# Kernel tuning notes

Measured on AMD Instinct MI355X. Metric: run time of the kernel, lower is better.

## Reference

```python
import jax, jax.numpy as jnp
import numpy as np

N, E, F_IN, HID, HEADS, NCLS, NG = 50000, 800000, 128, 128, 4, 10, 512
C = HID // HEADS          # per-head channels
BN_EPS = 1e-5
NEG_SLOPE = 0.2           # SuperGATConv default negative_slope
N_CONV = 3


def setup_inputs() -> dict:
    key = jax.random.key(0)
    ks = jax.random.split(key, 16)
    x = jax.random.normal(ks[0], (N, F_IN), jnp.float32)
    # edges with no self loops (reference appends self loops itself, as SuperGATConv does)
    src = jax.random.randint(ks[1], (E,), 0, N, dtype=jnp.int32)
    off = jax.random.randint(ks[2], (E,), 1, N, dtype=jnp.int32)
    dst = (src + off) % N
    edge_index = jnp.stack([src, dst], axis=0)
    batch = jnp.sort(jax.random.randint(ks[3], (N,), 0, NG, dtype=jnp.int32))
    s = 0.1
    # BatchNorm params per module init: weight=1, bias=1e-4 (running stats fresh: mean=0, var=1)
    inp = {
        "x": x, "edge_index": edge_index, "batch": batch,
        "bn_feat_g": jnp.ones((F_IN,), jnp.float32), "bn_feat_b": jnp.full((F_IN,), 1e-4, jnp.float32),
        "w_feat": jax.random.normal(ks[4], (F_IN, HID), jnp.float32) * s,
        "b_feat": jnp.zeros((HID,), jnp.float32),
        "bn_conv_g": jnp.ones((N_CONV, HID), jnp.float32), "bn_conv_b": jnp.full((N_CONV, HID), 1e-4, jnp.float32),
        "w_gat": jax.random.normal(ks[5], (N_CONV, HID, HID), jnp.float32) * s,
        "att_l": jax.random.normal(ks[6], (N_CONV, HEADS, C), jnp.float32) * s,
        "att_r": jax.random.normal(ks[7], (N_CONV, HEADS, C), jnp.float32) * s,
        "b_gat": jnp.zeros((N_CONV, HID), jnp.float32),
        "bn_fc_g": jnp.ones((HID,), jnp.float32), "bn_fc_b": jnp.full((HID,), 1e-4, jnp.float32),
        "w_fc": jax.random.normal(ks[8], (HID, HID), jnp.float32) * s,
        "b_fc": jnp.zeros((HID,), jnp.float32),
        "bn_hid_g": jnp.ones((HID,), jnp.float32), "bn_hid_b": jnp.full((HID,), 1e-4, jnp.float32),
        "w_cls": jax.random.normal(ks[9], (HID, NCLS), jnp.float32) * s,
        "b_cls": jnp.zeros((NCLS,), jnp.float32),
    }
    return inp


def _bn_eval(h, g, b):
    # eval-mode BatchNorm1d with fresh running stats (mean=0, var=1)
    return h * (g / jnp.sqrt(1.0 + BN_EPS)) + b


def _segment_softmax(a, seg, num_segments):
    # softmax over edges grouped by destination node (PyG softmax semantics)
    m = jax.ops.segment_max(a, seg, num_segments=num_segments)
    a = jnp.exp(a - m[seg])
    s = jax.ops.segment_sum(a, seg, num_segments=num_segments)
    return a / (s[seg] + 1e-16)


def _supergat_mx(h, src, dst, W, att_l, att_r, bias):
    # h: [N, HID] -> per-head features [N, H, C]
    hh = (h @ W).reshape(N, HEADS, C)
    h_j = hh[src]  # source (message) features  [E2, H, C]
    h_i = hh[dst]  # destination features       [E2, H, C]
    logits = jnp.einsum('ehc,ehc->eh', h_i, h_j)                       # MX dot-product
    alpha = jnp.einsum('ehc,hc->eh', h_j, att_l) + jnp.einsum('ehc,hc->eh', h_i, att_r)
    alpha = alpha * jax.nn.sigmoid(logits)
    alpha = jax.nn.leaky_relu(alpha, NEG_SLOPE)
    alpha = _segment_softmax(alpha, dst, N)                            # [E2, H]
    out = jax.ops.segment_sum(h_j * alpha[..., None], dst, num_segments=N)
    return out.reshape(N, HID) + bias


def reference(x, edge_index, batch, bn_feat_g, bn_feat_b, w_feat, b_feat,
              bn_conv_g, bn_conv_b, w_gat, att_l, att_r, b_gat,
              bn_fc_g, bn_fc_b, w_fc, b_fc, bn_hid_g, bn_hid_b, w_cls, b_cls):
    loops = jnp.arange(N, dtype=edge_index.dtype)
    src = jnp.concatenate([edge_index[0], loops])   # SuperGATConv adds self loops
    dst = jnp.concatenate([edge_index[1], loops])
    h = _bn_eval(x, bn_feat_g, bn_feat_b)
    h = jax.nn.relu(h @ w_feat + b_feat)            # GCNConv(gfn=True) == Linear
    for i in range(N_CONV):
        h = _bn_eval(h, bn_conv_g[i], bn_conv_b[i])
        h = jax.nn.relu(_supergat_mx(h, src, dst, w_gat[i], att_l[i], att_r[i], b_gat[i]))
    g = jax.ops.segment_sum(h, batch, num_segments=NG)  # global_add_pool -> [NG, HID]
    g = _bn_eval(g, bn_fc_g, bn_fc_b)
    g = jax.nn.relu(g @ w_fc + b_fc)
    g = _bn_eval(g, bn_hid_g, bn_hid_b)
    logits = g @ w_cls + b_cls
    att_loss = jnp.float32(0.0)  # eval mode: no edge-sampled attention loss
    return jax.nn.log_softmax(logits, axis=-1), att_loss
```

## Files before the change

### kernel.cpp

```cpp
#include <hip/hip_runtime.h>

#define NN 50000
#define EE 800000
#define FHID 128
#define NHEAD 4
#define NGRAPH 512
#define NCLS 10
#define BK 256
#define BCH 4096
#define NBLK_E 196
#define NBUCK 196
#define CAP 6144

typedef unsigned short u16;
typedef unsigned int u32;
typedef unsigned long long u64;
typedef __attribute__((ext_vector_type(8))) short bf16x8;
typedef __attribute__((ext_vector_type(4))) float f32x4;

__device__ __forceinline__ float bf2f(u16 u){
    union { u32 i; float f; } v; v.i = ((u32)u) << 16; return v.f;
}
__device__ __forceinline__ float bflo(u32 u){
    union { u32 i; float f; } v; v.i = u << 16; return v.f;
}
__device__ __forceinline__ float bfhi(u32 u){
    union { u32 i; float f; } v; v.i = u & 0xffff0000u; return v.f;
}
__device__ __forceinline__ u16 f2bf(float f){
    union { float f; u32 i; } v; v.f = f;
    u32 r = v.i + 0x7fffu + ((v.i >> 16) & 1u);
    return (u16)(r >> 16);
}
__device__ __forceinline__ u32 pack2(float a, float b){
    return ((u32)f2bf(b) << 16) | f2bf(a);
}
__device__ __forceinline__ float loadF(const void* p, int i, int isf32){
    return isf32 ? ((const float*)p)[i] : bf2f(((const u16*)p)[i]);
}
__device__ __forceinline__ void unpk8(uint4 v, float* f){
    f[0]=bflo(v.x); f[1]=bfhi(v.x);
    f[2]=bflo(v.y); f[3]=bfhi(v.y);
    f[4]=bflo(v.z); f[5]=bfhi(v.z);
    f[6]=bflo(v.w); f[7]=bfhi(v.w);
}

__global__ void detect_dtype(const u16* __restrict__ x, int* __restrict__ flag){
    __shared__ int cnt;
    if (threadIdx.x == 0) cnt = 0;
    __syncthreads();
    int ok = 0;
    for (int i = threadIdx.x; i < 1024; i += 256){
        u16 u = x[i];
        int e = (u >> 7) & 0xFF;
        if ((u & 0x7fff) == 0 || (e >= 0x70 && e <= 0x85)) ok++;
    }
    atomicAdd(&cnt, ok);
    __syncthreads();
    if (threadIdx.x == 0) flag[0] = (cnt < 900) ? 1 : 0;
}

__global__ void prep_weights(const void* __restrict__ w_feat, const void* __restrict__ b_feat,
                             const void* __restrict__ bn_feat_g, const void* __restrict__ bn_feat_b,
                             const void* __restrict__ w_gat, const void* __restrict__ bn_conv_g,
                             const void* __restrict__ bn_conv_b, const void* __restrict__ b_gat,
                             const int* __restrict__ flag,
                             u16* __restrict__ Wt, float* __restrict__ cvec,
                             float* __restrict__ biasv)
{
    __shared__ float red[128];
    int isf32 = flag[0];
    int L = blockIdx.x >> 7;
    int n = blockIdx.x & 127;
    int k = threadIdx.x;
    const float rs = rsqrtf(1.0f + 1e-5f);
    float wv, bg, bb;
    if (L == 0){
        wv = loadF(w_feat, k*FHID + n, isf32);
        bg = loadF(bn_feat_g, k, isf32);
        bb = loadF(bn_feat_b, k, isf32);
    } else {
        wv = loadF(w_gat, (L-1)*FHID*FHID + k*FHID + n, isf32);
        bg = loadF(bn_conv_g, (L-1)*FHID + k, isf32);
        bb = loadF(bn_conv_b, (L-1)*FHID + k, isf32);
    }
    Wt[L*FHID*FHID + n*FHID + k] = f2bf(bg * rs * wv);
    red[k] = bb * wv;
    __syncthreads();
    for (int o2 = 64; o2 > 0; o2 >>= 1){
        if (k < o2) red[k] += red[k + o2];
        __syncthreads();
    }
    if (k == 0){
        float c = red[0];
        if (L == 0) c += loadF(b_feat, n, isf32);
        cvec[L*FHID + n] = c;
        if (L > 0) biasv[L*FHID + n] = loadF(b_gat, (L-1)*FHID + n, isf32);
    }
}

__global__ void prep_head(const void* wfc, const void* bfc, const void* bnfg, const void* bnfb,
                          const void* bnhg, const void* bnhb, const void* wcls, const void* bcls,
                          const void* attl, const void* attr,
                          const int* __restrict__ flag, float* __restrict__ hp){
    int isf32 = flag[0];
    int gt = blockIdx.x*256 + threadIdx.x;
    for (int i = gt; i < FHID*FHID; i += 16*256) hp[i] = loadF(wfc, i, isf32);
    if (gt < FHID*NCLS) hp[16384 + gt] = loadF(wcls, gt, isf32);
    if (gt >= 2048 && gt < 2048 + 3*FHID){
        int i = gt - 2048;
        hp[18320 + i] = loadF(attl, i, isf32);
        hp[18704 + i] = loadF(attr, i, isf32);
    }
    if (gt >= 2560 && gt < 2560 + FHID){
        int t = gt - 2560;
        hp[17664 + t] = loadF(bnfg, t, isf32);
        hp[17792 + t] = loadF(bnfb, t, isf32);
        hp[17920 + t] = loadF(bfc,  t, isf32);
        hp[18048 + t] = loadF(bnhg, t, isf32);
        hp[18176 + t] = loadF(bnhb, t, isf32);
    }
    if (gt >= 3072 && gt < 3072 + NCLS) hp[18304 + (gt - 3072)] = loadF(bcls, gt - 3072, isf32);
}

__global__ __launch_bounds__(256) void gemm128(const void* __restrict__ A,
                                               const u16* __restrict__ Wt,
                                               const float* __restrict__ cvec,
                                               u16* __restrict__ out, int relu,
                                               int araw, const int* __restrict__ flag)
{
    int wave = threadIdx.x >> 6;
    int lane = threadIdx.x & 63;
    int m = lane & 15, quad = lane >> 4;
    int rowbase = blockIdx.x * 128 + wave * 32;
    bool f32in = araw && flag[0];
    const u16*  Au = (const u16*)A;
    const float* Af = (const float*)A;
    int r0 = rowbase + m, r1 = rowbase + 16 + m;
    bool v0 = r0 < NN, v1 = r1 < NN;
    f32x4 acc[2][8];
#pragma unroll
    for (int i = 0; i < 2; i++)
#pragma unroll
        for (int j = 0; j < 8; j++) acc[i][j] = (f32x4){0.f,0.f,0.f,0.f};
#pragma unroll
    for (int t = 0; t < 4; t++){
        bf16x8 a0 = {0,0,0,0,0,0,0,0}, a1 = {0,0,0,0,0,0,0,0};
        int kof = t*32 + quad*8;
        if (f32in){
            if (v0){
                const float* p = Af + (size_t)r0*FHID + kof;
                float4 u0 = *(const float4*)p, u1 = *(const float4*)(p+4);
                a0[0]=(short)f2bf(u0.x); a0[1]=(short)f2bf(u0.y);
                a0[2]=(short)f2bf(u0.z); a0[3]=(short)f2bf(u0.w);
                a0[4]=(short)f2bf(u1.x); a0[5]=(short)f2bf(u1.y);
                a0[6]=(short)f2bf(u1.z); a0[7]=(short)f2bf(u1.w);
            }
            if (v1){
                const float* p = Af + (size_t)r1*FHID + kof;
                float4 u0 = *(const float4*)p, u1 = *(const float4*)(p+4);
                a1[0]=(short)f2bf(u0.x); a1[1]=(short)f2bf(u0.y);
                a1[2]=(short)f2bf(u0.z); a1[3]=(short)f2bf(u0.w);
                a1[4]=(short)f2bf(u1.x); a1[5]=(short)f2bf(u1.y);
                a1[6]=(short)f2bf(u1.z); a1[7]=(short)f2bf(u1.w);
            }
        } else {
            if (v0) a0 = *(const bf16x8*)(Au + (size_t)r0*FHID + kof);
            if (v1) a1 = *(const bf16x8*)(Au + (size_t)r1*FHID + kof);
        }
#pragma unroll
        for (int ct = 0; ct < 8; ct++){
            bf16x8 wfrag = *(const bf16x8*)(Wt + (ct*16 + m)*FHID + kof);
            acc[0][ct] = __builtin_amdgcn_mfma_f32_16x16x32_bf16(wfrag, a0, acc[0][ct], 0, 0, 0);
            acc[1][ct] = __builtin_amdgcn_mfma_f32_16x16x32_bf16(wfrag, a1, acc[1][ct], 0, 0, 0);
        }
    }
#pragma unroll
    for (int tt = 0; tt < 2; tt++){
        int row = rowbase + tt*16 + m;
        if (row < NN){
#pragma unroll
            for (int ct = 0; ct < 8; ct++){
                int cb = ct*16 + quad*4;
                float4 cv = *(const float4*)(cvec + cb);
                float w0 = acc[tt][ct][0] + cv.x;
                float w1 = acc[tt][ct][1] + cv.y;
                float w2 = acc[tt][ct][2] + cv.z;
                float w3 = acc[tt][ct][3] + cv.w;
                if (relu){
                    w0 = fmaxf(w0, 0.f); w1 = fmaxf(w1, 0.f);
                    w2 = fmaxf(w2, 0.f); w3 = fmaxf(w3, 0.f);
                }
                uint2 st; st.x = pack2(w0, w1); st.y = pack2(w2, w3);
                *(uint2*)(out + (size_t)row*FHID + cb) = st;
            }
        }
    }
}

__global__ void node_alpha(const u16* __restrict__ hh, const float* __restrict__ attl,
                           const float* __restrict__ attr,
                           float* __restrict__ al, float* __restrict__ ar)
{
    int idx = blockIdx.x*blockDim.x + threadIdx.x;
    if (idx >= NN*NHEAD) return;
    int head = idx & 3;
    const u16* base = hh + (size_t)(idx >> 2)*FHID + head*32;
    float sl = 0.f, sr = 0.f;
#pragma unroll
    for (int v = 0; v < 4; v++){
        uint4 u = *(const uint4*)(base + v*8);
        float f[8]; unpk8(u, f);
#pragma unroll
        for (int j = 0; j < 8; j++){
            int c = head*32 + v*8 + j;
            sl += f[j] * attl[c];
            sr += f[j] * attr[c];
        }
    }
    al[idx] = sl; ar[idx] = sr;
}

__global__ __launch_bounds__(256) void bucket_hist(const int* __restrict__ dst,
                                                   int* __restrict__ gcnt){
    __shared__ int h[BK];
    int t = threadIdx.x;
    h[t] = 0;
    __syncthreads();
    int base = blockIdx.x * BCH;
#pragma unroll
    for (int k = 0; k < 16; k++){
        int e = base + k*256 + t;
        if (e < EE){
            u32 d = (u32)dst[e];
            if (d < NN) atomicAdd(&h[d >> 8], 1);
        }
    }
    __syncthreads();
    if (h[t]) atomicAdd(&gcnt[t], h[t]);
}

__global__ void bucket_scan(const int* __restrict__ gcnt, int* __restrict__ gbase,
                            int* __restrict__ gcur, int* __restrict__ rowst){
    __shared__ int sm[BK];
    int t = threadIdx.x;
    int v = gcnt[t];
    sm[t] = v;
    __syncthreads();
    for (int off = 1; off < BK; off <<= 1){
        int x = (t >= off) ? sm[t - off] : 0;
        __syncthreads();
        sm[t] += x;
        __syncthreads();
    }
    gbase[t] = sm[t] - v;
    gcur[t]  = sm[t] - v;
    if (t == BK - 1) rowst[NN] = sm[t];
}

__global__ __launch_bounds__(256) void bin_edges(const int* __restrict__ srcp,
        const int* __restrict__ dstp, int* __restrict__ gcur, u64* __restrict__ binned)
{
    __shared__ int h[BK], lb[BK], gb[BK], cur[BK];
    __shared__ u64 stage[BCH];
    int t = threadIdx.x;
    h[t] = 0;
    __syncthreads();
    int base = blockIdx.x * BCH;
    int sv[16], dv[16];
#pragma unroll
    for (int k = 0; k < 16; k++){
        int e = base + k*256 + t;
        int d = -1, s = 0;
        if (e < EE){
            d = dstp[e]; s = srcp[e];
            if ((u32)d >= NN) d = -1;
        }
        sv[k] = s; dv[k] = d;
        if (d >= 0) atomicAdd(&h[d >> 8], 1);
    }
    __syncthreads();
    lb[t] = h[t];
    __syncthreads();
    for (int off = 1; off < BK; off <<= 1){
        int x = (t >= off) ? lb[t - off] : 0;
        __syncthreads();
        lb[t] += x;
        __syncthreads();
    }
    int excl = lb[t] - h[t];
    int tot  = lb[BK-1];
    __syncthreads();
    lb[t] = excl;
    gb[t] = h[t] ? atomicAdd(&gcur[t], h[t]) : 0;
    cur[t] = 0;
    __syncthreads();
#pragma unroll
    for (int k = 0; k < 16; k++){
        int d = dv[k];
        if (d >= 0){
            int b = d >> 8;
            int p = lb[b] + atomicAdd(&cur[b], 1);
            stage[p] = ((u64)(u32)d << 32) | (u32)sv[k];
        }
    }
    __syncthreads();
    for (int i = t; i < tot; i += 256){
        u64 pr = stage[i];
        int b = (int)(pr >> 40);
        binned[gb[b] + (i - lb[b])] = pr;
    }
}

__global__ __launch_bounds__(256) void build_csr(const u64* __restrict__ binned,
        const int* __restrict__ gbase, const int* __restrict__ gcnt,
        int* __restrict__ rowst, int* __restrict__ colbuf)
{
    __shared__ int deg[BK], ls[BK], cur[BK];
    __shared__ int colstage[CAP];
    int b = blockIdx.x, t = threadIdx.x;
    int gb = gbase[b], cnt = gcnt[b];
    deg[t] = 0;
    __syncthreads();
    for (int i = t; i < cnt; i += 256){
        int d = (int)(binned[gb + i] >> 32);
        atomicAdd(&deg[d & 255], 1);
    }
    __syncthreads();
    ls[t] = deg[t];
    __syncthreads();
    for (int off = 1; off < BK; off <<= 1){
        int x = (t >= off) ? ls[t - off] : 0;
        __syncthreads();
        ls[t] += x;
        __syncthreads();
    }
    int excl = ls[t] - deg[t];
    int node = b*256 + t;
    if (node < NN) rowst[node] = gb + excl;
    cur[t] = excl;
    __syncthreads();
    for (int i = t; i < cnt; i += 256){
        u64 pr = binned[gb + i];
        int d = (int)(pr >> 32) & 255;
        int s = (int)(u32)pr;
        int p = atomicAdd(&cur[d], 1);
        if (p < CAP) colstage[p] = s;
        else colbuf[gb + p] = s;
    }
    __syncthreads();
    int mm = min(cnt, CAP);
    for (int i = t; i < mm; i += 256) colbuf[gb + i] = colstage[i];
}

__global__ __launch_bounds__(256) void supergat_conv(const u16* __restrict__ hh,
        const float* __restrict__ al, const float* __restrict__ ar,
        const int* __restrict__ rowstart, const int* __restrict__ colbuf,
        const float* __restrict__ bias, u16* __restrict__ hout)
{
    int wid  = (blockIdx.x*256 + threadIdx.x) >> 6;
    int lane = threadIdx.x & 63;
    int group = lane >> 4;
    int gl    = lane & 15;
    int head  = gl >> 2;
    int q     = gl & 3;
    int node  = wid*4 + group;
    bool valid = node < NN;
    int chbase = head*32 + q*8;
    int snode = valid ? node : 0;

    uint4 hdv = *(const uint4*)(hh + (size_t)snode*FHID + chbase);
    float hd[8]; unpk8(hdv, hd);
    float arn = ar[snode*NHEAD + head];
    float aln = al[snode*NHEAD + head];

    float d = hd[0]*hd[0]+hd[1]*hd[1]+hd[2]*hd[2]+hd[3]*hd[3]
            + hd[4]*hd[4]+hd[5]*hd[5]+hd[6]*hd[6]+hd[7]*hd[7];
    d += __shfl_xor(d, 1, 64);
    d += __shfl_xor(d, 2, 64);
    float a = (aln + arn) * (1.0f / (1.0f + __expf(-d)));
    a = (a > 0.0f) ? a : 0.2f*a;
    float p = __expf(fminf(a, 60.f));
    float s = p;
    float o[8];
#pragma unroll
    for (int i = 0; i < 8; i++) o[i] = p*hd[i];

    int e0 = valid ? rowstart[node]     : 0;
    int e1 = valid ? rowstart[node + 1] : 0;
    if (e0 < 0) e0 = 0;
    if (e1 > EE) e1 = EE;

    int e = e0;
    for (; e + 1 < e1; e += 2){
        int s1 = colbuf[e], s2 = colbuf[e + 1];
        if ((u32)s1 >= NN) s1 = 0;
        if ((u32)s2 >= NN) s2 = 0;
        uint4 x1 = *(const uint4*)(hh + (size_t)s1*FHID + chbase);
        uint4 x2 = *(const uint4*)(hh + (size_t)s2*FHID + chbase);
        float af1 = al[s1*NHEAD + head];
        float af2 = al[s2*NHEAD + head];
        float hs[8];
        unpk8(x1, hs);
        float lg = hd[0]*hs[0]+hd[1]*hs[1]+hd[2]*hs[2]+hd[3]*hs[3]
                 + hd[4]*hs[4]+hd[5]*hs[5]+hd[6]*hs[6]+hd[7]*hs[7];
        lg += __shfl_xor(lg, 1, 64);
        lg += __shfl_xor(lg, 2, 64);
        float a2 = (af1 + arn) * (1.0f / (1.0f + __expf(-lg)));
        a2 = (a2 > 0.0f) ? a2 : 0.2f*a2;
        float pe = __expf(fminf(a2, 60.f));
        s += pe;
#pragma unroll
        for (int i = 0; i < 8; i++) o[i] += pe*hs[i];
        unpk8(x2, hs);
        lg = hd[0]*hs[0]+hd[1]*hs[1]+hd[2]*hs[2]+hd[3]*hs[3]
           + hd[4]*hs[4]+hd[5]*hs[5]+hd[6]*hs[6]+hd[7]*hs[7];
        lg += __shfl_xor(lg, 1, 64);
        lg += __shfl_xor(lg, 2, 64);
        a2 = (af2 + arn) * (1.0f / (1.0f + __expf(-lg)));
        a2 = (a2 > 0.0f) ? a2 : 0.2f*a2;
        pe = __expf(fminf(a2, 60.f));
        s += pe;
#pragma unroll
        for (int i = 0; i < 8; i++) o[i] += pe*hs[i];
    }
    if (e < e1){
        int s1 = colbuf[e];
        if ((u32)s1 >= NN) s1 = 0;
        uint4 x1 = *(const uint4*)(hh + (size_t)s1*FHID + chbase);
        float af1 = al[s1*NHEAD + head];
        float hs[8]; unpk8(x1, hs);
        float lg = hd[0]*hs[0]+hd[1]*hs[1]+hd[2]*hs[2]+hd[3]*hs[3]
                 + hd[4]*hs[4]+hd[5]*hs[5]+hd[6]*hs[6]+hd[7]*hs[7];
        lg += __shfl_xor(lg, 1, 64);
        lg += __shfl_xor(lg, 2, 64);
        float a2 = (af1 + arn) * (1.0f / (1.0f + __expf(-lg)));
        a2 = (a2 > 0.0f) ? a2 : 0.2f*a2;
        float pe = __expf(fminf(a2, 60.f));
        s += pe;
#pragma unroll
        for (int i = 0; i < 8; i++) o[i] += pe*hs[i];
    }

    if (valid){
        float inv = 1.0f / (s + 1e-16f);
        uint4 w;
        w.x = pack2(fmaxf(o[0]*inv + bias[chbase+0], 0.f),
                    fmaxf(o[1]*inv + bias[chbase+1], 0.f));
        w.y = pack2(fmaxf(o[2]*inv + bias[chbase+2], 0.f),
                    fmaxf(o[3]*inv + bias[chbase+3], 0.f));
        w.z = pack2(fmaxf(o[4]*inv + bias[chbase+4], 0.f),
                    fmaxf(o[5]*inv + bias[chbase+5], 0.f));
        w.w = pack2(fmaxf(o[6]*inv + bias[chbase+6], 0.f),
                    fmaxf(o[7]*inv + bias[chbase+7], 0.f));
        *(uint4*)(hout + (size_t)node*FHID + chbase) = w;
    }
}

__global__ void pool_kernel(const u16* __restrict__ h, const int* __restrict__ batch,
                            float* __restrict__ g)
{
    __shared__ int bounds[2];
    int b = blockIdx.x, t = threadIdx.x;
    if (t < 2){
        int target = b + t;
        int lo = 0, hi = NN;
        while (lo < hi){
            int mid = (lo + hi) >> 1;
            if (batch[mid] < target) lo = mid + 1; else hi = mid;
        }
        bounds[t] = lo;
    }
    __syncthreads();
    float acc = 0.f;
    for (int node = bounds[0]; node < bounds[1]; node++)
        acc += bf2f(h[(size_t)node*FHID + t]);
    g[b*FHID + t] = acc;
}

__global__ void head_kernel(const float* __restrict__ g, const float* __restrict__ hp,
                            const int* __restrict__ flag, void* __restrict__ out)
{
    __shared__ float gb[FHID];
    __shared__ float g2[FHID];
    __shared__ float lg[16];
    int gi = blockIdx.x, t = threadIdx.x;
    int isf32 = flag[0];
    const float rs = rsqrtf(1.0f + 1e-5f);
    gb[t] = g[gi*FHID + t] * (hp[17664 + t] * rs) + hp[17792 + t];
    __syncthreads();
    float acc = hp[17920 + t];
    for (int k = 0; k < FHID; k++) acc += gb[k] * hp[k*FHID + t];
    acc = fmaxf(acc, 0.f);
    g2[t] = acc * (hp[18048 + t] * rs) + hp[18176 + t];
    __syncthreads();
    if (t < NCLS){
        float l = hp[18304 + t];
        for (int k = 0; k < FHID; k++) l += g2[k] * hp[16384 + k*NCLS + t];
        lg[t] = l;
    }
    __syncthreads();
    if (t == 0){
        float mx = lg[0];
        for (int j = 1; j < NCLS; j++) mx = fmaxf(mx, lg[j]);
        float se = 0.f;
        for (int j = 0; j < NCLS; j++) se += __expf(lg[j] - mx);
        float lse = logf(se) + mx;
        if (isf32){
            float* o = (float*)out;
            for (int j = 0; j < NCLS; j++) o[gi*NCLS + j] = lg[j] - lse;
            if (gi == 0) o[NGRAPH*NCLS] = 0.f;
        } else {
            u16* o = (u16*)out;
            for (int j = 0; j < NCLS; j++) o[gi*NCLS + j] = f2bf(lg[j] - lse);
            if (gi == 0) o[NGRAPH*NCLS] = 0;
        }
    }
}

extern "C" void kernel_launch(void* const* d_in, const int* in_sizes, int n_in,
                              void* d_out, int out_size, void* d_ws, size_t ws_size,
                              hipStream_t stream)
{
    (void)in_sizes; (void)n_in; (void)out_size; (void)ws_size;
    const void* x         = d_in[0];
    const int* edge       = (const int*)d_in[1];
    const int* batch      = (const int*)d_in[2];

    char* ws = (char*)d_ws;
    size_t off = 0;
    auto alloc = [&](size_t bytes) -> char* {
        char* p = ws + off; off += (bytes + 255) & ~(size_t)255; return p;
    };
    int*   dflag   = (int*)  alloc(256);
    u16*   WtAll   = (u16*)  alloc((size_t)4*FHID*FHID*2);
    float* cvecAll = (float*)alloc((size_t)4*FHID*4);
    float* biasv   = (float*)alloc((size_t)4*FHID*4);
    float* headp   = (float*)alloc((size_t)19088*4);
    float* al      = (float*)alloc((size_t)NN*NHEAD*4);
    float* ar      = (float*)alloc((size_t)NN*NHEAD*4);
    int*   rowst   = (int*)  alloc((size_t)(NN+1)*4);
    int*   gcnt    = (int*)  alloc((size_t)BK*4);
    int*   gbase   = (int*)  alloc((size_t)BK*4);
    int*   gcur    = (int*)  alloc((size_t)BK*4);
    float* g       = (float*)alloc((size_t)NGRAPH*FHID*4);
    int*   colbuf  = (int*)  alloc((size_t)EE*4);
    u16*   hA      = (u16*)  alloc((size_t)NN*FHID*2);
    u16*   hB      = (u16*)  alloc((size_t)NN*FHID*2);
    u64*   binned  = (u64*)hB;

    const int* srcp = edge;
    const int* dstp = edge + EE;

    detect_dtype<<<1, 256, 0, stream>>>((const u16*)x, dflag);
    prep_weights<<<512, 128, 0, stream>>>(d_in[5], d_in[6], d_in[3], d_in[4],
                                          d_in[9], d_in[7], d_in[8], d_in[12],
                                          dflag, WtAll, cvecAll, biasv);
    prep_head<<<16, 256, 0, stream>>>(d_in[15], d_in[16], d_in[13], d_in[14],
                                      d_in[17], d_in[18], d_in[19], d_in[20],
                                      d_in[10], d_in[11], dflag, headp);

    hipMemsetAsync(gcnt, 0, (size_t)BK*4, stream);
    bucket_hist<<<NBLK_E, 256, 0, stream>>>(dstp, gcnt);
    bucket_scan<<<1, 256, 0, stream>>>(gcnt, gbase, gcur, rowst);
    bin_edges<<<NBLK_E, 256, 0, stream>>>(srcp, dstp, gcur, binned);
    build_csr<<<NBUCK, 256, 0, stream>>>(binned, gbase, gcnt, rowst, colbuf);

    gemm128<<<(NN + 127)/128, 256, 0, stream>>>(x, WtAll, cvecAll, hA, 1, 1, dflag);

    for (int i = 0; i < 3; i++){
        gemm128<<<(NN + 127)/128, 256, 0, stream>>>(hA, WtAll + (i+1)*FHID*FHID,
                                                    cvecAll + (i+1)*FHID, hB, 0, 0, dflag);
        node_alpha<<<(NN*NHEAD + 255)/256, 256, 0, stream>>>(hB, headp + 18320 + i*FHID,
                                                             headp + 18704 + i*FHID, al, ar);
        supergat_conv<<<(NN + 15)/16, 256, 0, stream>>>(hB, al, ar, rowst, colbuf,
                                                        biasv + (i+1)*FHID, hA);
    }

    pool_kernel<<<NGRAPH, 128, 0, stream>>>(hA, batch, g);
    head_kernel<<<NGRAPH, 128, 0, stream>>>(g, headp, dflag, d_out);
}
```

Baseline: 429.5 us.

## Fuse attention logits into GEMM, degree-sort nodes, unroll gather, merge pool with head

The per-head attention dot products (al/ar) are now computed in the GEMM epilogue with cross-lane shuffles, which removes the separate node_alpha kernel and its re-read of the hidden features. Nodes are bucketed by in-degree through a small histogram, scan and scatter, and the conv kernel walks them in that order so the waves in a block see similar edge counts. The edge loop is unrolled by four so four neighbour loads are in flight together. Pooling and the classifier head are merged into one kernel, at the cost of three extra setup kernels and an indirection through perm.

```diff
diff --git a/kernel.cpp b/kernel.cpp
--- a/kernel.cpp
+++ b/kernel.cpp
@@ -127,7 +127,11 @@
                                                const u16* __restrict__ Wt,
                                                const float* __restrict__ cvec,
                                                u16* __restrict__ out, int relu,
-                                               int araw, const int* __restrict__ flag)
+                                               int araw, const int* __restrict__ flag,
+                                               const float* __restrict__ attl,
+                                               const float* __restrict__ attr,
+                                               float* __restrict__ al,
+                                               float* __restrict__ ar)
 {
     int wave = threadIdx.x >> 6;
     int lane = threadIdx.x & 63;
@@ -175,50 +179,51 @@
             acc[1][ct] = __builtin_amdgcn_mfma_f32_16x16x32_bf16(wfrag, a1, acc[1][ct], 0, 0, 0);
         }
     }
+    bool doa = (attl != nullptr);
 #pragma unroll
     for (int tt = 0; tt < 2; tt++){
         int row = rowbase + tt*16 + m;
-        if (row < NN){
-#pragma unroll
-            for (int ct = 0; ct < 8; ct++){
-                int cb = ct*16 + quad*4;
-                float4 cv = *(const float4*)(cvec + cb);
-                float w0 = acc[tt][ct][0] + cv.x;
-                float w1 = acc[tt][ct][1] + cv.y;
-                float w2 = acc[tt][ct][2] + cv.z;
-                float w3 = acc[tt][ct][3] + cv.w;
-                if (relu){
-                    w0 = fmaxf(w0, 0.f); w1 = fmaxf(w1, 0.f);
-                    w2 = fmaxf(w2, 0.f); w3 = fmaxf(w3, 0.f);
-                }
+        bool rv = row < NN;
+        float sl[4] = {0.f,0.f,0.f,0.f};
+        float sr[4] = {0.f,0.f,0.f,0.f};
+#pragma unroll
+        for (int ct = 0; ct < 8; ct++){
+            int cb = ct*16 + quad*4;
+            float4 cv = *(const float4*)(cvec + cb);
+            float w0 = acc[tt][ct][0] + cv.x;
+            float w1 = acc[tt][ct][1] + cv.y;
+            float w2 = acc[tt][ct][2] + cv.z;
+            float w3 = acc[tt][ct][3] + cv.w;
+            if (relu){
+                w0 = fmaxf(w0, 0.f); w1 = fmaxf(w1, 0.f);
+                w2 = fmaxf(w2, 0.f); w3 = fmaxf(w3, 0.f);
+            }
+            if (doa){
+                int h = ct >> 1;
+                float4 tl = *(const float4*)(attl + cb);
+                float4 tr = *(const float4*)(attr + cb);
+                sl[h] += w0*tl.x + w1*tl.y + w2*tl.z + w3*tl.w;
+                sr[h] += w0*tr.x + w1*tr.y + w2*tr.z + w3*tr.w;
+            }
+            if (rv){
                 uint2 st; st.x = pack2(w0, w1); st.y = pack2(w2, w3);
                 *(uint2*)(out + (size_t)row*FHID + cb) = st;
             }
         }
-    }
-}
-
-__global__ void node_alpha(const u16* __restrict__ hh, const float* __restrict__ attl,
-                           const float* __restrict__ attr,
-                           float* __restrict__ al, float* __restrict__ ar)
-{
-    int idx = blockIdx.x*blockDim.x + threadIdx.x;
-    if (idx >= NN*NHEAD) return;
-    int head = idx & 3;
-    const u16* base = hh + (size_t)(idx >> 2)*FHID + head*32;
-    float sl = 0.f, sr = 0.f;
-#pragma unroll
-    for (int v = 0; v < 4; v++){
-        uint4 u = *(const uint4*)(base + v*8);
-        float f[8]; unpk8(u, f);
-#pragma unroll
-        for (int j = 0; j < 8; j++){
-            int c = head*32 + v*8 + j;
-            sl += f[j] * attl[c];
-            sr += f[j] * attr[c];
-        }
-    }
-    al[idx] = sl; ar[idx] = sr;
+        if (doa){
+#pragma unroll
+            for (int h = 0; h < 4; h++){
+                sl[h] += __shfl_xor(sl[h], 16, 64);
+                sl[h] += __shfl_xor(sl[h], 32, 64);
+                sr[h] += __shfl_xor(sr[h], 16, 64);
+                sr[h] += __shfl_xor(sr[h], 32, 64);
+            }
+            if (rv){
+                al[row*NHEAD + quad] = sl[quad];
+                ar[row*NHEAD + quad] = sr[quad];
+            }
+        }
+    }
 }
 
 __global__ __launch_bounds__(256) void bucket_hist(const int* __restrict__ dst,
@@ -353,9 +358,43 @@
     for (int i = t; i < mm; i += 256) colbuf[gb + i] = colstage[i];
 }
 
+__global__ void deg_hist(const int* __restrict__ rowst, int* __restrict__ dhist){
+    int i = blockIdx.x*256 + threadIdx.x;
+    if (i < NN){
+        int d = rowst[i+1] - rowst[i];
+        d = (d < 0) ? 0 : ((d > 255) ? 255 : d);
+        atomicAdd(&dhist[d], 1);
+    }
+}
+__global__ void deg_scan(const int* __restrict__ dhist, int* __restrict__ dcur){
+    __shared__ int sm[256];
+    int t = threadIdx.x;
+    int v = dhist[t];
+    sm[t] = v;
+    __syncthreads();
+    for (int off = 1; off < 256; off <<= 1){
+        int x = (t >= off) ? sm[t - off] : 0;
+        __syncthreads();
+        sm[t] += x;
+        __syncthreads();
+    }
+    dcur[t] = sm[t] - v;
+}
+__global__ void deg_scatter(const int* __restrict__ rowst, int* __restrict__ dcur,
+                            int* __restrict__ perm){
+    int i = blockIdx.x*256 + threadIdx.x;
+    if (i < NN){
+        int d = rowst[i+1] - rowst[i];
+        d = (d < 0) ? 0 : ((d > 255) ? 255 : d);
+        int p = atomicAdd(&dcur[d], 1);
+        perm[p] = i;
+    }
+}
+
 __global__ __launch_bounds__(256) void supergat_conv(const u16* __restrict__ hh,
         const float* __restrict__ al, const float* __restrict__ ar,
         const int* __restrict__ rowstart, const int* __restrict__ colbuf,
+        const int* __restrict__ perm,
         const float* __restrict__ bias, u16* __restrict__ hout)
 {
     int wid  = (blockIdx.x*256 + threadIdx.x) >> 6;
@@ -364,15 +403,16 @@
     int gl    = lane & 15;
     int head  = gl >> 2;
     int q     = gl & 3;
-    int node  = wid*4 + group;
-    bool valid = node < NN;
+    int idx   = wid*4 + group;
+    bool valid = idx < NN;
+    int node = valid ? perm[idx] : 0;
+    if ((u32)node >= NN) node = 0;
     int chbase = head*32 + q*8;
-    int snode = valid ? node : 0;
-
-    uint4 hdv = *(const uint4*)(hh + (size_t)snode*FHID + chbase);
+
+    uint4 hdv = *(const uint4*)(hh + (size_t)node*FHID + chbase);
     float hd[8]; unpk8(hdv, hd);
-    float arn = ar[snode*NHEAD + head];
-    float aln = al[snode*NHEAD + head];
+    float arn = ar[node*NHEAD + head];
+    float aln = al[node*NHEAD + head];
 
     float d = hd[0]*hd[0]+hd[1]*hd[1]+hd[2]*hd[2]+hd[3]*hd[3]
             + hd[4]*hd[4]+hd[5]*hd[5]+hd[6]*hd[6]+hd[7]*hd[7];
@@ -392,43 +432,40 @@
     if (e1 > EE) e1 = EE;
 
     int e = e0;
-    for (; e + 1 < e1; e += 2){
-        int s1 = colbuf[e], s2 = colbuf[e + 1];
-        if ((u32)s1 >= NN) s1 = 0;
-        if ((u32)s2 >= NN) s2 = 0;
-        uint4 x1 = *(const uint4*)(hh + (size_t)s1*FHID + chbase);
-        uint4 x2 = *(const uint4*)(hh + (size_t)s2*FHID + chbase);
-        float af1 = al[s1*NHEAD + head];
-        float af2 = al[s2*NHEAD + head];
-        float hs[8];
-        unpk8(x1, hs);
-        float lg = hd[0]*hs[0]+hd[1]*hs[1]+hd[2]*hs[2]+hd[3]*hs[3]
-                 + hd[4]*hs[4]+hd[5]*hs[5]+hd[6]*hs[6]+hd[7]*hs[7];
-        lg += __shfl_xor(lg, 1, 64);
-        lg += __shfl_xor(lg, 2, 64);
-        float a2 = (af1 + arn) * (1.0f / (1.0f + __expf(-lg)));
-        a2 = (a2 > 0.0f) ? a2 : 0.2f*a2;
-        float pe = __expf(fminf(a2, 60.f));
-        s += pe;
-#pragma unroll
-        for (int i = 0; i < 8; i++) o[i] += pe*hs[i];
-        unpk8(x2, hs);
-        lg = hd[0]*hs[0]+hd[1]*hs[1]+hd[2]*hs[2]+hd[3]*hs[3]
-           + hd[4]*hs[4]+hd[5]*hs[5]+hd[6]*hs[6]+hd[7]*hs[7];
-        lg += __shfl_xor(lg, 1, 64);
-        lg += __shfl_xor(lg, 2, 64);
-        a2 = (af2 + arn) * (1.0f / (1.0f + __expf(-lg)));
-        a2 = (a2 > 0.0f) ? a2 : 0.2f*a2;
-        pe = __expf(fminf(a2, 60.f));
-        s += pe;
-#pragma unroll
-        for (int i = 0; i < 8; i++) o[i] += pe*hs[i];
-    }
-    if (e < e1){
-        int s1 = colbuf[e];
-        if ((u32)s1 >= NN) s1 = 0;
-        uint4 x1 = *(const uint4*)(hh + (size_t)s1*FHID + chbase);
-        float af1 = al[s1*NHEAD + head];
+    while (e + 3 < e1){
+        int sidx[4]; uint4 xv[4]; float af[4];
+#pragma unroll
+        for (int j = 0; j < 4; j++){
+            int si = colbuf[e + j];
+            if ((u32)si >= NN) si = 0;
+            sidx[j] = si;
+        }
+#pragma unroll
+        for (int j = 0; j < 4; j++){
+            xv[j] = *(const uint4*)(hh + (size_t)sidx[j]*FHID + chbase);
+            af[j] = al[sidx[j]*NHEAD + head];
+        }
+#pragma unroll
+        for (int j = 0; j < 4; j++){
+            float hs[8]; unpk8(xv[j], hs);
+            float lg = hd[0]*hs[0]+hd[1]*hs[1]+hd[2]*hs[2]+hd[3]*hs[3]
+                     + hd[4]*hs[4]+hd[5]*hs[5]+hd[6]*hs[6]+hd[7]*hs[7];
+            lg += __shfl_xor(lg, 1, 64);
+            lg += __shfl_xor(lg, 2, 64);
+            float a2 = (af[j] + arn) * (1.0f / (1.0f + __expf(-lg)));
+            a2 = (a2 > 0.0f) ? a2 : 0.2f*a2;
+            float pe = __expf(fminf(a2, 60.f));
+            s += pe;
+#pragma unroll
+            for (int i = 0; i < 8; i++) o[i] += pe*hs[i];
+        }
+        e += 4;
+    }
+    while (e < e1){
+        int si = colbuf[e];
+        if ((u32)si >= NN) si = 0;
+        uint4 x1 = *(const uint4*)(hh + (size_t)si*FHID + chbase);
+        float af1 = al[si*NHEAD + head];
         float hs[8]; unpk8(x1, hs);
         float lg = hd[0]*hs[0]+hd[1]*hs[1]+hd[2]*hs[2]+hd[3]*hs[3]
                  + hd[4]*hs[4]+hd[5]*hs[5]+hd[6]*hs[6]+hd[7]*hs[7];
@@ -440,6 +477,7 @@
         s += pe;
 #pragma unroll
         for (int i = 0; i < 8; i++) o[i] += pe*hs[i];
+        e++;
     }
 
     if (valid){
@@ -457,37 +495,31 @@
     }
 }
 
-__global__ void pool_kernel(const u16* __restrict__ h, const int* __restrict__ batch,
-                            float* __restrict__ g)
+__global__ void pool_head(const u16* __restrict__ h, const int* __restrict__ batch,
+                          const float* __restrict__ hp, const int* __restrict__ flag,
+                          void* __restrict__ out)
 {
     __shared__ int bounds[2];
-    int b = blockIdx.x, t = threadIdx.x;
-    if (t < 2){
-        int target = b + t;
-        int lo = 0, hi = NN;
-        while (lo < hi){
-            int mid = (lo + hi) >> 1;
-            if (batch[mid] < target) lo = mid + 1; else hi = mid;
-        }
-        bounds[t] = lo;
-    }
-    __syncthreads();
-    float acc = 0.f;
-    for (int node = bounds[0]; node < bounds[1]; node++)
-        acc += bf2f(h[(size_t)node*FHID + t]);
-    g[b*FHID + t] = acc;
-}
-
-__global__ void head_kernel(const float* __restrict__ g, const float* __restrict__ hp,
-                            const int* __restrict__ flag, void* __restrict__ out)
-{
     __shared__ float gb[FHID];
     __shared__ float g2[FHID];
     __shared__ float lg[16];
     int gi = blockIdx.x, t = threadIdx.x;
     int isf32 = flag[0];
+    if (t < 2){
+        int target = gi + t;
+        int lo = 0, hi = NN;
+        while (lo < hi){
+            int mid = (lo + hi) >> 1;
+            if (batch[mid] < target) lo = mid + 1; else hi = mid;
+        }
+        bounds[t] = lo;
+    }
+    __syncthreads();
+    float acc0 = 0.f;
+    for (int node = bounds[0]; node < bounds[1]; node++)
+        acc0 += bf2f(h[(size_t)node*FHID + t]);
     const float rs = rsqrtf(1.0f + 1e-5f);
-    gb[t] = g[gi*FHID + t] * (hp[17664 + t] * rs) + hp[17792 + t];
+    gb[t] = acc0 * (hp[17664 + t] * rs) + hp[17792 + t];
     __syncthreads();
     float acc = hp[17920 + t];
     for (int k = 0; k < FHID; k++) acc += gb[k] * hp[k*FHID + t];
@@ -543,7 +575,9 @@
     int*   gcnt    = (int*)  alloc((size_t)BK*4);
     int*   gbase   = (int*)  alloc((size_t)BK*4);
     int*   gcur    = (int*)  alloc((size_t)BK*4);
-    float* g       = (float*)alloc((size_t)NGRAPH*FHID*4);
+    int*   dhist   = (int*)  alloc((size_t)256*4);
+    int*   dcur    = (int*)  alloc((size_t)256*4);
+    int*   perm    = (int*)  alloc((size_t)NN*4);
     int*   colbuf  = (int*)  alloc((size_t)EE*4);
     u16*   hA      = (u16*)  alloc((size_t)NN*FHID*2);
     u16*   hB      = (u16*)  alloc((size_t)NN*FHID*2);
@@ -551,6 +585,7 @@
 
     const int* srcp = edge;
     const int* dstp = edge + EE;
+    const int NB_N = (NN + 255)/256;
 
     detect_dtype<<<1, 256, 0, stream>>>((const u16*)x, dflag);
     prep_weights<<<512, 128, 0, stream>>>(d_in[5], d_in[6], d_in[3], d_in[4],
@@ -561,22 +596,26 @@
                                       d_in[10], d_in[11], dflag, headp);
 
     hipMemsetAsync(gcnt, 0, (size_t)BK*4, stream);
+    hipMemsetAsync(dhist, 0, (size_t)256*4, stream);
     bucket_hist<<<NBLK_E, 256, 0, stream>>>(dstp, gcnt);
     bucket_scan<<<1, 256, 0, stream>>>(gcnt, gbase, gcur, rowst);
     bin_edges<<<NBLK_E, 256, 0, stream>>>(srcp, dstp, gcur, binned);
     build_csr<<<NBUCK, 256, 0, stream>>>(binned, gbase, gcnt, rowst, colbuf);
-
-    gemm128<<<(NN + 127)/128, 256, 0, stream>>>(x, WtAll, cvecAll, hA, 1, 1, dflag);
+    deg_hist<<<NB_N, 256, 0, stream>>>(rowst, dhist);
+    deg_scan<<<1, 256, 0, stream>>>(dhist, dcur);
+    deg_scatter<<<NB_N, 256, 0, stream>>>(rowst, dcur, perm);
+
+    gemm128<<<(NN + 127)/128, 256, 0, stream>>>(x, WtAll, cvecAll, hA, 1, 1, dflag,
+                                                nullptr, nullptr, nullptr, nullptr);
 
     for (int i = 0; i < 3; i++){
         gemm128<<<(NN + 127)/128, 256, 0, stream>>>(hA, WtAll + (i+1)*FHID*FHID,
-                                                    cvecAll + (i+1)*FHID, hB, 0, 0, dflag);
-        node_alpha<<<(NN*NHEAD + 255)/256, 256, 0, stream>>>(hB, headp + 18320 + i*FHID,
-                                                             headp + 18704 + i*FHID, al, ar);
-        supergat_conv<<<(NN + 15)/16, 256, 0, stream>>>(hB, al, ar, rowst, colbuf,
+                                                    cvecAll + (i+1)*FHID, hB, 0, 0, dflag,
+                                                    headp + 18320 + i*FHID,
+                                                    headp + 18704 + i*FHID, al, ar);
+        supergat_conv<<<(NN + 15)/16, 256, 0, stream>>>(hB, al, ar, rowst, colbuf, perm,
                                                         biasv + (i+1)*FHID, hA);
     }
 
-    pool_kernel<<<NGRAPH, 128, 0, stream>>>(hA, batch, g);
-    head_kernel<<<NGRAPH, 128, 0, stream>>>(g, headp, dflag, d_out);
-}
+    pool_head<<<NGRAPH, 128, 0, stream>>>(hA, batch, headp, dflag, d_out);
+}
```

Result: slower. 682.9 us (+59.0%).
